# Kernel tuning notes

Hardware: AMD Instinct MI355X
Metric: run time of the kernel (lower is better)

The kernel has to match this reference:

```python
import jax, jax.numpy as jnp
import numpy as np

N = 50000      # nodes
E = 1_600_000  # edges per metapath graph
M = 3          # meta-path patterns
D = 128        # feature dim (in_size == out_size, GraphConv has no weight)
H = 128        # semantic-attention hidden size


def setup_inputs() -> dict:
    key = jax.random.key(0)
    k1, k2, k3, k4 = jax.random.split(key, 4)
    h = jax.random.normal(k1, (N, D), dtype=jnp.float32)
    # edges[m, 0] = src node ids, edges[m, 1] = dst node ids for metapath m
    edges = jax.random.randint(k2, (M, 2, E), 0, N, dtype=jnp.int32)
    W1 = jax.random.normal(k3, (D, H), dtype=jnp.float32) * 0.05
    b1 = jnp.zeros((H,), dtype=jnp.float32)
    W2 = jax.random.normal(k4, (H, 1), dtype=jnp.float32) * 0.05
    return {"h": h, "edges": edges, "W1": W1, "b1": b1, "W2": W2}


def _graph_conv_both(h, src, dst, n):
    """DGL GraphConv(norm='both', weight=None, bias=None):
    out = D_in^{-1/2} * A @ (D_out^{-1/2} * h), zero degrees clamped to 1."""
    ones = jnp.ones_like(src, dtype=h.dtype)
    out_deg = jax.ops.segment_sum(ones, src, num_segments=n)
    in_deg = jax.ops.segment_sum(ones, dst, num_segments=n)
    norm_src = jax.lax.rsqrt(jnp.maximum(out_deg, 1.0))
    norm_dst = jax.lax.rsqrt(jnp.maximum(in_deg, 1.0))
    msg = (h * norm_src[:, None])[src]                  # [E, D] gather
    agg = jax.ops.segment_sum(msg, dst, num_segments=n)  # [N, D] scatter-add
    return agg * norm_dst[:, None]


def reference(h, edges, W1, b1, W2):
    n = h.shape[0]
    m = edges.shape[0]
    # One normalized sparse aggregation per meta-path (fixed small M).
    z = jnp.stack(
        [_graph_conv_both(h, edges[i, 0], edges[i, 1], n) for i in range(m)],
        axis=1,
    )  # [N, M, D]
    # Semantic attention: project -> tanh -> score, mean over nodes, softmax over M.
    w = jnp.mean(jnp.tanh(z @ W1 + b1) @ W2, axis=0)  # [M, 1]
    beta = jax.nn.softmax(w, axis=0)                  # [M, 1]
    return jnp.sum(beta[None, :, :] * z, axis=1)      # [N, D]
```

## Files before the change

kernel.cpp:

```cpp
#include <hip/hip_runtime.h>
#include <cstdint>
#include <cstddef>

typedef unsigned int  uint;
typedef unsigned short ushort;
typedef short bf16x8 __attribute__((ext_vector_type(8)));
typedef float f32x4  __attribute__((ext_vector_type(4)));

#define N_NODES 50000
#define N_EDGES 1600000
#define N_META  3
#define DIM     128

#define BKT       256
#define NBKT      196
#define CSR_CAP   10240
#define OCH       128
#define EPC       (N_EDGES / OCH)
#define OWORDS    12500
#define PREP_A    (N_META * OCH)
#define W1C_B     4
#define SCALE_B   6250

#define AT_TILE   64
#define AT_NBLK   782

__device__ __forceinline__ uint bf16rne(float f) {
    const uint u = __float_as_uint(f);
    return (u + 0x7FFFu + ((u >> 16) & 1u)) >> 16;
}
__device__ __forceinline__ float bflo(uint p) { return __uint_as_float(p << 16); }
__device__ __forceinline__ float bfhi(uint p) { return __uint_as_float(p & 0xFFFF0000u); }
__device__ __forceinline__ float fast_tanh(float x) {
    const float e = __expf(2.0f * x);
    return 1.0f - 2.0f / (e + 1.0f);
}

__global__ __launch_bounds__(256) void prep_kernel(
        const int* __restrict__ edges, const float* __restrict__ W1,
        uint* __restrict__ bhout, int* __restrict__ bucket_cnt,
        uint* __restrict__ partials, ushort* __restrict__ W1T) {
    __shared__ __align__(16) uint sh[OWORDS];
    __shared__ uint bh[NBKT];
    const int blk = blockIdx.x;
    if (blk < PREP_A) {
        const int m = blk >> 7, c = blk & 127;
        uint4* sh4 = reinterpret_cast<uint4*>(sh);
        for (int j = threadIdx.x; j < OWORDS / 4; j += 256)
            sh4[j] = make_uint4(0u, 0u, 0u, 0u);
        for (int j = threadIdx.x; j < NBKT; j += 256) bh[j] = 0;
        __syncthreads();
        const int* src = edges + (size_t)(2 * m) * N_EDGES;
        const int* dst = edges + (size_t)(2 * m + 1) * N_EDGES;
        const int beg = c * EPC;
        for (int i = beg + 4 * threadIdx.x; i + 4 <= beg + EPC; i += 1024) {
            const uint4 s4 = *reinterpret_cast<const uint4*>(src + i);
            const uint4 d4 = *reinterpret_cast<const uint4*>(dst + i);
            atomicAdd(&sh[s4.x >> 2], 1u << (8 * (s4.x & 3)));
            atomicAdd(&sh[s4.y >> 2], 1u << (8 * (s4.y & 3)));
            atomicAdd(&sh[s4.z >> 2], 1u << (8 * (s4.z & 3)));
            atomicAdd(&sh[s4.w >> 2], 1u << (8 * (s4.w & 3)));
            atomicAdd(&bh[d4.x >> 8], 1u);
            atomicAdd(&bh[d4.y >> 8], 1u);
            atomicAdd(&bh[d4.z >> 8], 1u);
            atomicAdd(&bh[d4.w >> 8], 1u);
        }
        __syncthreads();
        uint4* outp4 = reinterpret_cast<uint4*>(
            partials + (size_t)(m * OCH + c) * OWORDS);
        for (int j = threadIdx.x; j < OWORDS / 4; j += 256) outp4[j] = sh4[j];
        uint* bo = bhout + (size_t)(m * OCH + c) * NBKT;
        for (int j = threadIdx.x; j < NBKT; j += 256) {
            const uint v = bh[j];
            bo[j] = v;
            if (v) atomicAdd(&bucket_cnt[m * NBKT + j], (int)v);
        }
    } else {
        const int base = (blk - PREP_A) * (DIM * DIM / W1C_B);
        for (int o = base + threadIdx.x; o < base + DIM * DIM / W1C_B; o += 256) {
            const int j = o >> 7, k = o & 127;
            W1T[o] = (ushort)bf16rne(W1[k * DIM + j]);
        }
    }
}

__global__ __launch_bounds__(256) void scan_nsrc_kernel(
        const int* __restrict__ bucket_cnt, int* __restrict__ bucket_off,
        int* __restrict__ row_off, const uint* __restrict__ partials,
        float* __restrict__ nsrc) {
    const int blk = blockIdx.x;
    if (blk < N_META) {
        __shared__ int sc[256];
        const int m = blk, t = threadIdx.x;
        const int v = (t < NBKT) ? bucket_cnt[m * NBKT + t] : 0;
        sc[t] = v;
        __syncthreads();
        for (int off = 1; off < 256; off <<= 1) {
            const int tt = (t >= off) ? sc[t - off] : 0;
            __syncthreads();
            sc[t] += tt;
            __syncthreads();
        }
        const int excl = sc[t] - v;
        if (t < NBKT) bucket_off[m * (NBKT + 1) + t] = excl;
        if (t == 0) {
            bucket_off[m * (NBKT + 1) + NBKT] = N_EDGES;
            row_off[m * (N_NODES + 1) + N_NODES] = N_EDGES;
        }
    } else {
        const int i = (blk - N_META) * 256 + threadIdx.x;
        if (i < N_META * N_NODES) {
            const int m = i / N_NODES, node = i - m * N_NODES;
            const int q = node >> 2, s8 = 8 * (node & 3);
            int s = 0;
#pragma unroll 8
            for (int c = 0; c < OCH; ++c)
                s += (partials[(size_t)(m * OCH + c) * OWORDS + q] >> s8) & 0xFF;
            nsrc[i] = rsqrtf(fmaxf((float)s, 1.0f));
        }
    }
}

__global__ __launch_bounds__(256) void bin_scale_kernel(
        const int* __restrict__ edges, const uint* __restrict__ bhout,
        const int* __restrict__ bucket_off, const float* __restrict__ h,
        const float* __restrict__ nsrc, uint* __restrict__ pairs,
        ushort* __restrict__ hbm) {
    const int blk = blockIdx.x;
    if (blk < PREP_A) {
        const int m = blk >> 7, c = blk & 127;
        __shared__ int cur[NBKT];
        for (int j = threadIdx.x; j < NBKT; j += 256) {
            int base = bucket_off[m * (NBKT + 1) + j];
            for (int cc = 0; cc < c; ++cc)
                base += (int)bhout[(size_t)(m * OCH + cc) * NBKT + j];
            cur[j] = base;
        }
        __syncthreads();
        const int* src = edges + (size_t)(2 * m) * N_EDGES;
        const int* dst = edges + (size_t)(2 * m + 1) * N_EDGES;
        const int beg = c * EPC;
        uint* pm = pairs + (size_t)m * N_EDGES;
        for (int i = beg + 4 * threadIdx.x; i + 4 <= beg + EPC; i += 1024) {
            const uint4 s4 = *reinterpret_cast<const uint4*>(src + i);
            const uint4 d4 = *reinterpret_cast<const uint4*>(dst + i);
            int p0 = atomicAdd(&cur[d4.x >> 8], 1);
            pm[p0] = (d4.x << 16) | s4.x;
            int p1 = atomicAdd(&cur[d4.y >> 8], 1);
            pm[p1] = (d4.y << 16) | s4.y;
            int p2 = atomicAdd(&cur[d4.z >> 8], 1);
            pm[p2] = (d4.z << 16) | s4.z;
            int p3 = atomicAdd(&cur[d4.w >> 8], 1);
            pm[p3] = (d4.w << 16) | s4.w;
        }
    } else {
        const int i = (blk - PREP_A) * 256 + threadIdx.x;
        const int node = i >> 5;
        const float4 v = reinterpret_cast<const float4*>(h)[i];
        uint2* o = reinterpret_cast<uint2*>(hbm);
#pragma unroll
        for (int m = 0; m < N_META; ++m) {
            const float n = nsrc[m * N_NODES + node];
            uint2 p;
            p.x = bf16rne(v.x * n) | (bf16rne(v.y * n) << 16);
            p.y = bf16rne(v.z * n) | (bf16rne(v.w * n) << 16);
            o[(size_t)m * (N_NODES * DIM / 4) + i] = p;
        }
    }
}

__global__ __launch_bounds__(256) void csr_kernel(
        const uint* __restrict__ pairs, const int* __restrict__ bucket_off,
        int* __restrict__ row_off, ushort* __restrict__ csr) {
    const int b = blockIdx.x, m = blockIdx.y;
    const int node_base = b * BKT;
    const int nb = min(BKT, N_NODES - node_base);
    __shared__ uint stage[CSR_CAP];
    __shared__ int hist[BKT];
    __shared__ int sc[BKT];
    __shared__ int cur[BKT];
    hist[threadIdx.x] = 0;
    __syncthreads();
    const int beg = bucket_off[m * (NBKT + 1) + b];
    const int end = bucket_off[m * (NBKT + 1) + b + 1];
    const int cnt = end - beg;
    const uint* pm = pairs + (size_t)m * N_EDGES + beg;
    for (int i = threadIdx.x; i < cnt; i += 256) {
        const uint p = pm[i];
        if (i < CSR_CAP) stage[i] = p;
        atomicAdd(&hist[(int)(p >> 16) - node_base], 1);
    }
    __syncthreads();
    const int v = hist[threadIdx.x];
    sc[threadIdx.x] = v;
    __syncthreads();
    for (int off = 1; off < BKT; off <<= 1) {
        const int t = (threadIdx.x >= off) ? sc[threadIdx.x - off] : 0;
        __syncthreads();
        sc[threadIdx.x] += t;
        __syncthreads();
    }
    const int excl = sc[threadIdx.x] - v;
    cur[threadIdx.x] = beg + excl;
    if (threadIdx.x < nb)
        row_off[m * (N_NODES + 1) + node_base + threadIdx.x] = beg + excl;
    __syncthreads();
    ushort* cm = csr + (size_t)m * N_EDGES;
    for (int i = threadIdx.x; i < cnt; i += 256) {
        const uint p = (i < CSR_CAP) ? stage[i] : pm[i];
        const int dl = (int)(p >> 16) - node_base;
        const int pos = atomicAdd(&cur[dl], 1);
        cm[pos] = (ushort)(p & 0xFFFFu);
    }
}

__global__ __launch_bounds__(256) void gather_kernel(
        const ushort* __restrict__ hbm, const ushort* __restrict__ csr,
        const int* __restrict__ row_off, ushort* __restrict__ zb) {
    const int m    = blockIdx.y;
    const int wave = threadIdx.x >> 6;
    const int lane = threadIdx.x & 63;
    const int q    = lane >> 4;
    const int c16  = lane & 15;
    const int node = blockIdx.x * 4 + wave;
    const int* ro = row_off + m * (N_NODES + 1);
    const int beg = ro[node];
    const int end = ro[node + 1];
    const ushort* srcs = csr + (size_t)m * N_EDGES;
    const ushort* tab  = hbm + (size_t)m * N_NODES * DIM;
    float acc[8] = {};
    int j = beg;
    for (; j + 16 <= end; j += 16) {
        int s[4]; uint4 hv[4];
#pragma unroll
        for (int u = 0; u < 4; ++u) s[u] = srcs[j + 4 * u + q];
#pragma unroll
        for (int u = 0; u < 4; ++u)
            hv[u] = *reinterpret_cast<const uint4*>(tab + (size_t)s[u] * DIM + c16 * 8);
#pragma unroll
        for (int u = 0; u < 4; ++u) {
            acc[0] += bflo(hv[u].x); acc[1] += bfhi(hv[u].x);
            acc[2] += bflo(hv[u].y); acc[3] += bfhi(hv[u].y);
            acc[4] += bflo(hv[u].z); acc[5] += bfhi(hv[u].z);
            acc[6] += bflo(hv[u].w); acc[7] += bfhi(hv[u].w);
        }
    }
    for (; j + 4 <= end; j += 4) {
        const int s0 = srcs[j + q];
        const uint4 hv = *reinterpret_cast<const uint4*>(tab + (size_t)s0 * DIM + c16 * 8);
        acc[0] += bflo(hv.x); acc[1] += bfhi(hv.x);
        acc[2] += bflo(hv.y); acc[3] += bfhi(hv.y);
        acc[4] += bflo(hv.z); acc[5] += bfhi(hv.z);
        acc[6] += bflo(hv.w); acc[7] += bfhi(hv.w);
    }
    if (j + q < end) {
        const int s0 = srcs[j + q];
        const uint4 hv = *reinterpret_cast<const uint4*>(tab + (size_t)s0 * DIM + c16 * 8);
        acc[0] += bflo(hv.x); acc[1] += bfhi(hv.x);
        acc[2] += bflo(hv.y); acc[3] += bfhi(hv.y);
        acc[4] += bflo(hv.z); acc[5] += bfhi(hv.z);
        acc[6] += bflo(hv.w); acc[7] += bfhi(hv.w);
    }
#pragma unroll
    for (int k = 0; k < 8; ++k) {
        acc[k] += __shfl_xor(acc[k], 16);
        acc[k] += __shfl_xor(acc[k], 32);
    }
    if (lane < 16) {
        const float nd = rsqrtf(fmaxf((float)(end - beg), 1.0f));
        uint4 o;
        o.x = bf16rne(acc[0] * nd) | (bf16rne(acc[1] * nd) << 16);
        o.y = bf16rne(acc[2] * nd) | (bf16rne(acc[3] * nd) << 16);
        o.z = bf16rne(acc[4] * nd) | (bf16rne(acc[5] * nd) << 16);
        o.w = bf16rne(acc[6] * nd) | (bf16rne(acc[7] * nd) << 16);
        *reinterpret_cast<uint4*>(
            zb + ((size_t)m * N_NODES + node) * DIM + c16 * 8) = o;
    }
}

__global__ __launch_bounds__(256) void attn_kernel(
        const ushort* __restrict__ zb, const ushort* __restrict__ W1T,
        const float* __restrict__ b1, const float* __restrict__ W2,
        float* __restrict__ wacc) {
    const int m   = blockIdx.y;
    const int tid = threadIdx.x;
    const int wv  = tid >> 6;
    const int l   = tid & 63;
    __shared__ __align__(16) ushort w1s[DIM * DIM];
    __shared__ float red[4];

    {
        const uint4* g = reinterpret_cast<const uint4*>(W1T);
        for (int i = tid; i < DIM * DIM / 8; i += 256) {
            const int j = i >> 4;
            const int slot = i ^ (j & 7);
            *reinterpret_cast<uint4*>(
                reinterpret_cast<char*>(w1s) + slot * 16) = g[i];
        }
    }
    __syncthreads();

    const int node_base = blockIdx.x * AT_TILE + wv * 16;
    const int row = l & 15;
    const int q   = l >> 4;
    int nload = node_base + row;
    if (nload >= N_NODES) nload = N_NODES - 1;
    const ushort* zrow = zb + ((size_t)m * N_NODES + nload) * DIM + q * 8;

    bf16x8 a[4];
#pragma unroll
    for (int kk = 0; kk < 4; ++kk)
        a[kk] = *reinterpret_cast<const bf16x8*>(zrow + kk * 32);

    f32x4 acc[8];
#pragma unroll
    for (int ct = 0; ct < 8; ++ct) acc[ct] = (f32x4){0.f, 0.f, 0.f, 0.f};

#pragma unroll
    for (int kk = 0; kk < 4; ++kk) {
#pragma unroll
        for (int ct = 0; ct < 8; ++ct) {
            const int j = ct * 16 + row;
            const int slot = (j * 16 + kk * 4 + q) ^ (j & 7);
            const bf16x8 b = *reinterpret_cast<const bf16x8*>(
                reinterpret_cast<char*>(w1s) + slot * 16);
            acc[ct] = __builtin_amdgcn_mfma_f32_16x16x32_bf16(
                a[kk], b, acc[ct], 0, 0, 0);
        }
    }

    float local = 0.0f;
#pragma unroll
    for (int ct = 0; ct < 8; ++ct) {
        const int j = ct * 16 + row;
        const float b1j = b1[j];
        const float w2j = W2[j];
#pragma unroll
        for (int r = 0; r < 4; ++r) {
            const int nd = node_base + q * 4 + r;
            if (nd < N_NODES)
                local += fast_tanh(acc[ct][r] + b1j) * w2j;
        }
    }
    for (int off = 32; off > 0; off >>= 1)
        local += __shfl_xor(local, off);
    if (l == 0) red[wv] = local;
    __syncthreads();
    if (tid == 0)
        atomicAdd(&wacc[m], red[0] + red[1] + red[2] + red[3]);
}

__global__ __launch_bounds__(256) void final_kernel(
        const ushort* __restrict__ zb, const float* __restrict__ wacc,
        float* __restrict__ out) {
    const int g = blockIdx.x * 256 + threadIdx.x;
    const float invN = 1.0f / (float)N_NODES;
    const float w0 = wacc[0] * invN, w1 = wacc[1] * invN, w2 = wacc[2] * invN;
    const float mx = fmaxf(w0, fmaxf(w1, w2));
    const float e0 = expf(w0 - mx), e1 = expf(w1 - mx), e2 = expf(w2 - mx);
    const float inv = 1.0f / (e0 + e1 + e2);
    const float beta[3] = {e0 * inv, e1 * inv, e2 * inv};
    float a[8] = {};
#pragma unroll
    for (int m = 0; m < N_META; ++m) {
        const uint4 v = reinterpret_cast<const uint4*>(zb)[
            (size_t)m * (N_NODES * DIM / 8) + g];
        const float bm = beta[m];
        a[0] = fmaf(bflo(v.x), bm, a[0]); a[1] = fmaf(bfhi(v.x), bm, a[1]);
        a[2] = fmaf(bflo(v.y), bm, a[2]); a[3] = fmaf(bfhi(v.y), bm, a[3]);
        a[4] = fmaf(bflo(v.z), bm, a[4]); a[5] = fmaf(bfhi(v.z), bm, a[5]);
        a[6] = fmaf(bflo(v.w), bm, a[6]); a[7] = fmaf(bfhi(v.w), bm, a[7]);
    }
    float4 o0 = {a[0], a[1], a[2], a[3]};
    float4 o1 = {a[4], a[5], a[6], a[7]};
    reinterpret_cast<float4*>(out)[(size_t)g * 2 + 0] = o0;
    reinterpret_cast<float4*>(out)[(size_t)g * 2 + 1] = o1;
}

extern "C" void kernel_launch(void* const* d_in, const int* in_sizes, int n_in,
                              void* d_out, int out_size, void* d_ws, size_t ws_size,
                              hipStream_t stream) {
    const float* h    = (const float*)d_in[0];
    const int*  edges = (const int*)d_in[1];
    const float* W1   = (const float*)d_in[2];
    const float* b1   = (const float*)d_in[3];
    const float* W2   = (const float*)d_in[4];
    float* out = (float*)d_out;

    char* p = (char*)d_ws;
    ushort* zb      = (ushort*)p;
    uint*  pairs    = (uint*)p;
    uint*  partials = (uint*)(p + (size_t)N_META * N_EDGES * 4);
    p += (size_t)N_META * N_NODES * DIM * 2;
    ushort* hbm     = (ushort*)p; p += (size_t)N_META * N_NODES * DIM * 2;
    ushort* csr     = (ushort*)p; p += (size_t)N_META * N_EDGES * 2;
    int* row_off    = (int*)p;    p += ((size_t)N_META * (N_NODES + 1) + 1) * 4;
    float* nsrc     = (float*)p;  p += (size_t)N_META * N_NODES * 4;
    float* wacc     = (float*)p;  p += 16 * 4;
    int* bucket_cnt = (int*)p;    p += (size_t)N_META * NBKT * 4;
    int* bucket_off = (int*)p;    p += (size_t)N_META * (NBKT + 1) * 4 + 4;
    uint* bhout     = (uint*)p;   p += (size_t)N_META * OCH * NBKT * 4;
    ushort* W1T     = (ushort*)p; p += (size_t)DIM * DIM * 2;

    hipMemsetAsync(wacc, 0, (16 + (size_t)N_META * NBKT) * 4, stream);

    prep_kernel<<<dim3(PREP_A + W1C_B), 256, 0, stream>>>(
        edges, W1, bhout, bucket_cnt, partials, W1T);
    scan_nsrc_kernel<<<dim3(N_META + (N_META * N_NODES + 255) / 256), 256, 0, stream>>>(
        bucket_cnt, bucket_off, row_off, partials, nsrc);
    bin_scale_kernel<<<dim3(PREP_A + SCALE_B), 256, 0, stream>>>(
        edges, bhout, bucket_off, h, nsrc, pairs, hbm);
    csr_kernel<<<dim3(NBKT, N_META), 256, 0, stream>>>(pairs, bucket_off, row_off, csr);
    gather_kernel<<<dim3(N_NODES / 4, N_META), 256, 0, stream>>>(
        hbm, csr, row_off, zb);
    attn_kernel<<<dim3(AT_NBLK, N_META), 256, 0, stream>>>(zb, W1T, b1, W2, wacc);
    final_kernel<<<dim3(N_NODES * DIM / 8 / 256), 256, 0, stream>>>(zb, wacc, out);
}
```

Baseline: 373.7 us.

## Pad CSR rows to 8-aligned slots and vectorize gather index loads

```diff
diff --git a/kernel.cpp b/kernel.cpp
--- a/kernel.cpp
+++ b/kernel.cpp
@@ -15,6 +15,8 @@
 #define BKT       256
 #define NBKT      196
 #define CSR_CAP   10240
+#define PBKT      11264
+#define CSRM      (NBKT * PBKT)
 #define OCH       128
 #define EPC       (N_EDGES / OCH)
 #define OWORDS    12500
@@ -86,8 +88,7 @@
 
 __global__ __launch_bounds__(256) void scan_nsrc_kernel(
         const int* __restrict__ bucket_cnt, int* __restrict__ bucket_off,
-        int* __restrict__ row_off, const uint* __restrict__ partials,
-        float* __restrict__ nsrc) {
+        const uint* __restrict__ partials, float* __restrict__ nsrc) {
     const int blk = blockIdx.x;
     if (blk < N_META) {
         __shared__ int sc[256];
@@ -103,10 +104,7 @@
         }
         const int excl = sc[t] - v;
         if (t < NBKT) bucket_off[m * (NBKT + 1) + t] = excl;
-        if (t == 0) {
-            bucket_off[m * (NBKT + 1) + NBKT] = N_EDGES;
-            row_off[m * (N_NODES + 1) + N_NODES] = N_EDGES;
-        }
+        if (t == 0) bucket_off[m * (NBKT + 1) + NBKT] = N_EDGES;
     } else {
         const int i = (blk - N_META) * 256 + threadIdx.x;
         if (i < N_META * N_NODES) {
@@ -171,7 +169,8 @@
 
 __global__ __launch_bounds__(256) void csr_kernel(
         const uint* __restrict__ pairs, const int* __restrict__ bucket_off,
-        int* __restrict__ row_off, ushort* __restrict__ csr) {
+        int* __restrict__ row_off, int* __restrict__ row_deg,
+        ushort* __restrict__ csr) {
     const int b = blockIdx.x, m = blockIdx.y;
     const int node_base = b * BKT;
     const int nb = min(BKT, N_NODES - node_base);
@@ -192,7 +191,8 @@
     }
     __syncthreads();
     const int v = hist[threadIdx.x];
-    sc[threadIdx.x] = v;
+    const int pd = (v + 7) & ~7;
+    sc[threadIdx.x] = pd;
     __syncthreads();
     for (int off = 1; off < BKT; off <<= 1) {
         const int t = (threadIdx.x >= off) ? sc[threadIdx.x - off] : 0;
@@ -200,12 +200,14 @@
         sc[threadIdx.x] += t;
         __syncthreads();
     }
-    const int excl = sc[threadIdx.x] - v;
-    cur[threadIdx.x] = beg + excl;
-    if (threadIdx.x < nb)
-        row_off[m * (N_NODES + 1) + node_base + threadIdx.x] = beg + excl;
-    __syncthreads();
-    ushort* cm = csr + (size_t)m * N_EDGES;
+    const int base = b * PBKT + (sc[threadIdx.x] - pd);
+    cur[threadIdx.x] = base;
+    if (threadIdx.x < nb) {
+        row_off[m * N_NODES + node_base + threadIdx.x] = base;
+        row_deg[m * N_NODES + node_base + threadIdx.x] = v;
+    }
+    __syncthreads();
+    ushort* cm = csr + (size_t)m * CSRM;
     for (int i = threadIdx.x; i < cnt; i += 256) {
         const uint p = (i < CSR_CAP) ? stage[i] : pm[i];
         const int dl = (int)(p >> 16) - node_base;
@@ -216,24 +218,46 @@
 
 __global__ __launch_bounds__(256) void gather_kernel(
         const ushort* __restrict__ hbm, const ushort* __restrict__ csr,
-        const int* __restrict__ row_off, ushort* __restrict__ zb) {
+        const int* __restrict__ row_off, const int* __restrict__ row_deg,
+        ushort* __restrict__ zb) {
     const int m    = blockIdx.y;
     const int wave = threadIdx.x >> 6;
     const int lane = threadIdx.x & 63;
     const int q    = lane >> 4;
     const int c16  = lane & 15;
     const int node = blockIdx.x * 4 + wave;
-    const int* ro = row_off + m * (N_NODES + 1);
-    const int beg = ro[node];
-    const int end = ro[node + 1];
-    const ushort* srcs = csr + (size_t)m * N_EDGES;
+    const int beg = row_off[m * N_NODES + node];
+    const int deg = row_deg[m * N_NODES + node];
+    const int end = beg + deg;
+    const ushort* srcs = csr + (size_t)m * CSRM;
     const ushort* tab  = hbm + (size_t)m * N_NODES * DIM;
     float acc[8] = {};
     int j = beg;
+    for (; j + 32 <= end; j += 32) {
+        const uint4 sp = *reinterpret_cast<const uint4*>(srcs + j + 8 * q);
+        int s[8];
+        s[0] = sp.x & 0xFFFF; s[1] = sp.x >> 16;
+        s[2] = sp.y & 0xFFFF; s[3] = sp.y >> 16;
+        s[4] = sp.z & 0xFFFF; s[5] = sp.z >> 16;
+        s[6] = sp.w & 0xFFFF; s[7] = sp.w >> 16;
+        uint4 hv[8];
+#pragma unroll
+        for (int u = 0; u < 8; ++u)
+            hv[u] = *reinterpret_cast<const uint4*>(tab + (size_t)s[u] * DIM + c16 * 8);
+#pragma unroll
+        for (int u = 0; u < 8; ++u) {
+            acc[0] += bflo(hv[u].x); acc[1] += bfhi(hv[u].x);
+            acc[2] += bflo(hv[u].y); acc[3] += bfhi(hv[u].y);
+            acc[4] += bflo(hv[u].z); acc[5] += bfhi(hv[u].z);
+            acc[6] += bflo(hv[u].w); acc[7] += bfhi(hv[u].w);
+        }
+    }
     for (; j + 16 <= end; j += 16) {
-        int s[4]; uint4 hv[4];
-#pragma unroll
-        for (int u = 0; u < 4; ++u) s[u] = srcs[j + 4 * u + q];
+        const uint2 sp = *reinterpret_cast<const uint2*>(srcs + j + 4 * q);
+        int s[4];
+        s[0] = sp.x & 0xFFFF; s[1] = sp.x >> 16;
+        s[2] = sp.y & 0xFFFF; s[3] = sp.y >> 16;
+        uint4 hv[4];
 #pragma unroll
         for (int u = 0; u < 4; ++u)
             hv[u] = *reinterpret_cast<const uint4*>(tab + (size_t)s[u] * DIM + c16 * 8);
@@ -267,7 +291,7 @@
         acc[k] += __shfl_xor(acc[k], 32);
     }
     if (lane < 16) {
-        const float nd = rsqrtf(fmaxf((float)(end - beg), 1.0f));
+        const float nd = rsqrtf(fmaxf((float)deg, 1.0f));
         uint4 o;
         o.x = bf16rne(acc[0] * nd) | (bf16rne(acc[1] * nd) << 16);
         o.y = bf16rne(acc[2] * nd) | (bf16rne(acc[3] * nd) << 16);
@@ -393,8 +417,9 @@
     uint*  partials = (uint*)(p + (size_t)N_META * N_EDGES * 4);
     p += (size_t)N_META * N_NODES * DIM * 2;
     ushort* hbm     = (ushort*)p; p += (size_t)N_META * N_NODES * DIM * 2;
-    ushort* csr     = (ushort*)p; p += (size_t)N_META * N_EDGES * 2;
-    int* row_off    = (int*)p;    p += ((size_t)N_META * (N_NODES + 1) + 1) * 4;
+    ushort* csr     = (ushort*)p; p += (size_t)N_META * CSRM * 2;
+    int* row_off    = (int*)p;    p += (size_t)N_META * N_NODES * 4;
+    int* row_deg    = (int*)p;    p += (size_t)N_META * N_NODES * 4;
     float* nsrc     = (float*)p;  p += (size_t)N_META * N_NODES * 4;
     float* wacc     = (float*)p;  p += 16 * 4;
     int* bucket_cnt = (int*)p;    p += (size_t)N_META * NBKT * 4;
@@ -407,12 +432,13 @@
     prep_kernel<<<dim3(PREP_A + W1C_B), 256, 0, stream>>>(
         edges, W1, bhout, bucket_cnt, partials, W1T);
     scan_nsrc_kernel<<<dim3(N_META + (N_META * N_NODES + 255) / 256), 256, 0, stream>>>(
-        bucket_cnt, bucket_off, row_off, partials, nsrc);
+        bucket_cnt, bucket_off, partials, nsrc);
     bin_scale_kernel<<<dim3(PREP_A + SCALE_B), 256, 0, stream>>>(
         edges, bhout, bucket_off, h, nsrc, pairs, hbm);
-    csr_kernel<<<dim3(NBKT, N_META), 256, 0, stream>>>(pairs, bucket_off, row_off, csr);
+    csr_kernel<<<dim3(NBKT, N_META), 256, 0, stream>>>(
+        pairs, bucket_off, row_off, row_deg, csr);
     gather_kernel<<<dim3(N_NODES / 4, N_META), 256, 0, stream>>>(
-        hbm, csr, row_off, zb);
+        hbm, csr, row_off, row_deg, zb);
     attn_kernel<<<dim3(AT_NBLK, N_META), 256, 0, stream>>>(zb, W1T, b1, W2, wacc);
     final_kernel<<<dim3(N_NODES * DIM / 8 / 256), 256, 0, stream>>>(zb, wacc, out);
 }
```

Result: no change. 376.6 us (+0.8%).

## Fold bucket scan and source-norm computation into bin_scale and csr kernels

Applied to the files above, without the earlier changes.

```diff
diff --git a/kernel.cpp b/kernel.cpp
--- a/kernel.cpp
+++ b/kernel.cpp
@@ -84,14 +84,17 @@
     }
 }
 
-__global__ __launch_bounds__(256) void scan_nsrc_kernel(
-        const int* __restrict__ bucket_cnt, int* __restrict__ bucket_off,
-        int* __restrict__ row_off, const uint* __restrict__ partials,
-        float* __restrict__ nsrc) {
+__global__ __launch_bounds__(256) void bin_scale_kernel(
+        const int* __restrict__ edges, const uint* __restrict__ bhout,
+        const int* __restrict__ bucket_cnt, const uint* __restrict__ partials,
+        const float* __restrict__ h, uint* __restrict__ pairs,
+        ushort* __restrict__ hbm) {
     const int blk = blockIdx.x;
-    if (blk < N_META) {
+    if (blk < PREP_A) {
+        const int m = blk >> 7, c = blk & 127;
         __shared__ int sc[256];
-        const int m = blk, t = threadIdx.x;
+        __shared__ int cur[NBKT];
+        const int t = threadIdx.x;
         const int v = (t < NBKT) ? bucket_cnt[m * NBKT + t] : 0;
         sc[t] = v;
         __syncthreads();
@@ -101,47 +104,18 @@
             sc[t] += tt;
             __syncthreads();
         }
-        const int excl = sc[t] - v;
-        if (t < NBKT) bucket_off[m * (NBKT + 1) + t] = excl;
-        if (t == 0) {
-            bucket_off[m * (NBKT + 1) + NBKT] = N_EDGES;
-            row_off[m * (N_NODES + 1) + N_NODES] = N_EDGES;
-        }
-    } else {
-        const int i = (blk - N_META) * 256 + threadIdx.x;
-        if (i < N_META * N_NODES) {
-            const int m = i / N_NODES, node = i - m * N_NODES;
-            const int q = node >> 2, s8 = 8 * (node & 3);
-            int s = 0;
-#pragma unroll 8
-            for (int c = 0; c < OCH; ++c)
-                s += (partials[(size_t)(m * OCH + c) * OWORDS + q] >> s8) & 0xFF;
-            nsrc[i] = rsqrtf(fmaxf((float)s, 1.0f));
-        }
-    }
-}
-
-__global__ __launch_bounds__(256) void bin_scale_kernel(
-        const int* __restrict__ edges, const uint* __restrict__ bhout,
-        const int* __restrict__ bucket_off, const float* __restrict__ h,
-        const float* __restrict__ nsrc, uint* __restrict__ pairs,
-        ushort* __restrict__ hbm) {
-    const int blk = blockIdx.x;
-    if (blk < PREP_A) {
-        const int m = blk >> 7, c = blk & 127;
-        __shared__ int cur[NBKT];
-        for (int j = threadIdx.x; j < NBKT; j += 256) {
-            int base = bucket_off[m * (NBKT + 1) + j];
+        if (t < NBKT) {
+            int base = sc[t] - v;
             for (int cc = 0; cc < c; ++cc)
-                base += (int)bhout[(size_t)(m * OCH + cc) * NBKT + j];
-            cur[j] = base;
+                base += (int)bhout[(size_t)(m * OCH + cc) * NBKT + t];
+            cur[t] = base;
         }
         __syncthreads();
         const int* src = edges + (size_t)(2 * m) * N_EDGES;
         const int* dst = edges + (size_t)(2 * m + 1) * N_EDGES;
         const int beg = c * EPC;
         uint* pm = pairs + (size_t)m * N_EDGES;
-        for (int i = beg + 4 * threadIdx.x; i + 4 <= beg + EPC; i += 1024) {
+        for (int i = beg + 4 * t; i + 4 <= beg + EPC; i += 1024) {
             const uint4 s4 = *reinterpret_cast<const uint4*>(src + i);
             const uint4 d4 = *reinterpret_cast<const uint4*>(dst + i);
             int p0 = atomicAdd(&cur[d4.x >> 8], 1);
@@ -154,13 +128,38 @@
             pm[p3] = (d4.w << 16) | s4.w;
         }
     } else {
-        const int i = (blk - PREP_A) * 256 + threadIdx.x;
-        const int node = i >> 5;
+        const int blk2 = blk - PREP_A;
+        const int tid = threadIdx.x;
+        __shared__ float snsrc[24];
+        if (tid < 192) {
+            const int wid = tid >> 5;
+            const int mm = wid >> 1, qi = wid & 1;
+            const int q = blk2 * 2 + qi;
+            const int l = tid & 31;
+            uint ws = 0;
+#pragma unroll
+            for (int k = 0; k < 4; ++k)
+                ws += partials[(size_t)(mm * OCH + l + 32 * k) * OWORDS + q];
+            ws += __shfl_xor(ws, 16);
+            ws += __shfl_xor(ws, 8);
+            ws += __shfl_xor(ws, 4);
+            ws += __shfl_xor(ws, 2);
+            ws += __shfl_xor(ws, 1);
+            if (l == 0) {
+#pragma unroll
+                for (int b = 0; b < 4; ++b)
+                    snsrc[mm * 8 + qi * 4 + b] =
+                        rsqrtf(fmaxf((float)((ws >> (8 * b)) & 0xFFu), 1.0f));
+            }
+        }
+        __syncthreads();
+        const int i = blk2 * 256 + tid;
+        const int nl = (i >> 5) & 7;
         const float4 v = reinterpret_cast<const float4*>(h)[i];
         uint2* o = reinterpret_cast<uint2*>(hbm);
 #pragma unroll
         for (int m = 0; m < N_META; ++m) {
-            const float n = nsrc[m * N_NODES + node];
+            const float n = snsrc[m * 8 + nl];
             uint2 p;
             p.x = bf16rne(v.x * n) | (bf16rne(v.y * n) << 16);
             p.y = bf16rne(v.z * n) | (bf16rne(v.w * n) << 16);
@@ -170,7 +169,7 @@
 }
 
 __global__ __launch_bounds__(256) void csr_kernel(
-        const uint* __restrict__ pairs, const int* __restrict__ bucket_off,
+        const uint* __restrict__ pairs, const int* __restrict__ bucket_cnt,
         int* __restrict__ row_off, ushort* __restrict__ csr) {
     const int b = blockIdx.x, m = blockIdx.y;
     const int node_base = b * BKT;
@@ -179,34 +178,50 @@
     __shared__ int hist[BKT];
     __shared__ int sc[BKT];
     __shared__ int cur[BKT];
-    hist[threadIdx.x] = 0;
-    __syncthreads();
-    const int beg = bucket_off[m * (NBKT + 1) + b];
-    const int end = bucket_off[m * (NBKT + 1) + b + 1];
+    __shared__ int bo2[2];
+    const int t = threadIdx.x;
+    {
+        const int v0 = (t < NBKT) ? bucket_cnt[m * NBKT + t] : 0;
+        sc[t] = v0;
+        __syncthreads();
+        for (int off = 1; off < 256; off <<= 1) {
+            const int tt = (t >= off) ? sc[t - off] : 0;
+            __syncthreads();
+            sc[t] += tt;
+            __syncthreads();
+        }
+        if (t == b) { bo2[0] = sc[t] - v0; bo2[1] = sc[t]; }
+    }
+    hist[t] = 0;
+    __syncthreads();
+    const int beg = bo2[0];
+    const int end = bo2[1];
     const int cnt = end - beg;
     const uint* pm = pairs + (size_t)m * N_EDGES + beg;
-    for (int i = threadIdx.x; i < cnt; i += 256) {
+    for (int i = t; i < cnt; i += 256) {
         const uint p = pm[i];
         if (i < CSR_CAP) stage[i] = p;
         atomicAdd(&hist[(int)(p >> 16) - node_base], 1);
     }
     __syncthreads();
-    const int v = hist[threadIdx.x];
-    sc[threadIdx.x] = v;
+    const int v = hist[t];
+    sc[t] = v;
     __syncthreads();
     for (int off = 1; off < BKT; off <<= 1) {
-        const int t = (threadIdx.x >= off) ? sc[threadIdx.x - off] : 0;
-        __syncthreads();
-        sc[threadIdx.x] += t;
-        __syncthreads();
-    }
-    const int excl = sc[threadIdx.x] - v;
-    cur[threadIdx.x] = beg + excl;
-    if (threadIdx.x < nb)
-        row_off[m * (N_NODES + 1) + node_base + threadIdx.x] = beg + excl;
+        const int tt = (t >= off) ? sc[t - off] : 0;
+        __syncthreads();
+        sc[t] += tt;
+        __syncthreads();
+    }
+    const int excl = sc[t] - v;
+    cur[t] = beg + excl;
+    if (t < nb)
+        row_off[m * (N_NODES + 1) + node_base + t] = beg + excl;
+    if (b == NBKT - 1 && t == 0)
+        row_off[m * (N_NODES + 1) + N_NODES] = N_EDGES;
     __syncthreads();
     ushort* cm = csr + (size_t)m * N_EDGES;
-    for (int i = threadIdx.x; i < cnt; i += 256) {
+    for (int i = t; i < cnt; i += 256) {
         const uint p = (i < CSR_CAP) ? stage[i] : pm[i];
         const int dl = (int)(p >> 16) - node_base;
         const int pos = atomicAdd(&cur[dl], 1);
@@ -395,10 +410,8 @@
     ushort* hbm     = (ushort*)p; p += (size_t)N_META * N_NODES * DIM * 2;
     ushort* csr     = (ushort*)p; p += (size_t)N_META * N_EDGES * 2;
     int* row_off    = (int*)p;    p += ((size_t)N_META * (N_NODES + 1) + 1) * 4;
-    float* nsrc     = (float*)p;  p += (size_t)N_META * N_NODES * 4;
     float* wacc     = (float*)p;  p += 16 * 4;
     int* bucket_cnt = (int*)p;    p += (size_t)N_META * NBKT * 4;
-    int* bucket_off = (int*)p;    p += (size_t)N_META * (NBKT + 1) * 4 + 4;
     uint* bhout     = (uint*)p;   p += (size_t)N_META * OCH * NBKT * 4;
     ushort* W1T     = (ushort*)p; p += (size_t)DIM * DIM * 2;
 
@@ -406,11 +419,10 @@
 
     prep_kernel<<<dim3(PREP_A + W1C_B), 256, 0, stream>>>(
         edges, W1, bhout, bucket_cnt, partials, W1T);
-    scan_nsrc_kernel<<<dim3(N_META + (N_META * N_NODES + 255) / 256), 256, 0, stream>>>(
-        bucket_cnt, bucket_off, row_off, partials, nsrc);
     bin_scale_kernel<<<dim3(PREP_A + SCALE_B), 256, 0, stream>>>(
-        edges, bhout, bucket_off, h, nsrc, pairs, hbm);
-    csr_kernel<<<dim3(NBKT, N_META), 256, 0, stream>>>(pairs, bucket_off, row_off, csr);
+        edges, bhout, bucket_cnt, partials, h, pairs, hbm);
+    csr_kernel<<<dim3(NBKT, N_META), 256, 0, stream>>>(
+        pairs, bucket_cnt, row_off, csr);
     gather_kernel<<<dim3(N_NODES / 4, N_META), 256, 0, stream>>>(
         hbm, csr, row_off, zb);
     attn_kernel<<<dim3(AT_NBLK, N_META), 256, 0, stream>>>(zb, W1T, b1, W2, wacc);
```

Measured after the change: 391.6 us. 4.8% more time.
